# Kernel tuning notes

Measured on AMD Instinct MI355X. Metric: run time of the kernel, lower is better.

## Reference

```python
import jax, jax.numpy as jnp
import numpy as np

N_NODES = 50000
N_EDGES = 1600000
HIDDEN = 128
IN_DIM = 3  # x (1) + relative pos (2)


def setup_inputs() -> dict:
    key = jax.random.key(0)
    ks = jax.random.split(key, 5)
    x = jax.random.normal(ks[0], (N_NODES, 1), dtype=jnp.float32)
    pos = jax.random.normal(ks[1], (N_NODES, 2), dtype=jnp.float32)
    # MLP params (Linear(3,128) -> ReLU -> Linear(128,128)), fan-in scaled
    W1 = jax.random.normal(ks[2], (IN_DIM, HIDDEN), dtype=jnp.float32) / np.sqrt(IN_DIM)
    b1 = jnp.zeros((HIDDEN,), dtype=jnp.float32)
    W2 = jax.random.normal(ks[3], (HIDDEN, HIDDEN), dtype=jnp.float32) / np.sqrt(HIDDEN)
    b2 = jnp.zeros((HIDDEN,), dtype=jnp.float32)
    edge_index = jax.random.randint(ks[4], (2, N_EDGES), 0, N_NODES, dtype=jnp.int64)
    return {"x": x, "pos": pos, "W1": W1, "b1": b1, "W2": W2, "b2": b2,
            "edge_index": edge_index}


def reference(x, pos, W1, b1, W2, b2, edge_index):
    # PTConv with aggr='add': per-edge message = nn(cat([x_j, pos_j - pos_i]))
    # then scatter-add into destination node i.
    src = edge_index[0]  # j (neighbor / source)
    dst = edge_index[1]  # i (center / destination)
    msg_in = jnp.concatenate([x[src], pos[src] - pos[dst]], axis=-1)  # [E, 3]
    h = jax.nn.relu(msg_in @ W1 + b1) @ W2 + b2                        # [E, 128]
    out = jax.ops.segment_sum(h, dst, num_segments=x.shape[0])        # [N, 128]
    return out
```

## Files before the change

kernel.cpp:

```cpp
#include <hip/hip_runtime.h>


#define HIDDEN 128
#define BNODES 32
#define SUPSH 10
#define CAPA 36864
#define CAPF 1536
#define EPBA 2048
#define KSUB 16
#define CAP 1536
#define W2LD 136

typedef float v2f __attribute__((ext_vector_type(2)));
typedef short bf16x8 __attribute__((ext_vector_type(8)));
typedef float f32x4 __attribute__((ext_vector_type(4)));

__device__ __forceinline__ unsigned short f2bf(float f) {
    unsigned int u = __float_as_uint(f);
    u += 0x7fffu + ((u >> 16) & 1u);
    return (unsigned short)(u >> 16);
}

__global__ void k_init(int* __restrict__ bcurA, int* __restrict__ bcurF,
                       int NSUP, int NB) {
    int i = blockIdx.x * blockDim.x + threadIdx.x;
    if (i < NSUP) bcurA[i] = i * CAPA;
    if (i < NB)   bcurF[i] = i * CAPF;
}

__global__ __launch_bounds__(256) void k_scatA(const int* __restrict__ src,
                                               const int* __restrict__ dst,
                                               int* __restrict__ bcurA,
                                               unsigned int* __restrict__ pairsA,
                                               int E, int NSUP) {
    __shared__ int h[64];
    __shared__ int hb[64];
    int tid = threadIdx.x;
    if (tid < 64) h[tid] = 0;
    __syncthreads();
    int base = blockIdx.x * EPBA;
    int lim = base + EPBA; if (lim > E) lim = E;
    for (int i = base + tid; i < lim; i += 256) atomicAdd(&h[dst[i] >> SUPSH], 1);
    __syncthreads();
    if (tid < NSUP) {
        int c = h[tid];
        hb[tid] = c ? atomicAdd(&bcurA[tid], c) : 0;
        h[tid] = 0;
    }
    __syncthreads();
    for (int i = base + tid; i < lim; i += 256) {
        int d = dst[i];
        int s = d >> SUPSH;
        int loc = atomicAdd(&h[s], 1);
        int slot = hb[s] + loc;
        if (slot < (s + 1) * CAPA)
            pairsA[slot] = ((unsigned int)src[i] << SUPSH) | (unsigned int)(d & 1023);
    }
}

__global__ __launch_bounds__(256) void k_scatB(const int* __restrict__ bcurA,
                                               const unsigned int* __restrict__ pairsA,
                                               int* __restrict__ bcurF,
                                               unsigned int* __restrict__ pairsF,
                                               int NB) {
    __shared__ int h[32];
    __shared__ int hb[32];
    int tid = threadIdx.x;
    int s = blockIdx.x / KSUB;
    int k = blockIdx.x % KSUB;
    int base0 = s * CAPA;
    int ec = bcurA[s] - base0; if (ec > CAPA) ec = CAPA;
    int slice = (ec + KSUB - 1) / KSUB;
    int lo = base0 + k * slice;
    int hi = lo + slice; { int e1 = base0 + ec; if (hi > e1) hi = e1; }
    if (tid < 32) h[tid] = 0;
    __syncthreads();
    for (int i = lo + tid; i < hi; i += 256) atomicAdd(&h[(pairsA[i] >> 5) & 31u], 1);
    __syncthreads();
    if (tid < 32) {
        int c = h[tid];
        hb[tid] = c ? atomicAdd(&bcurF[s * 32 + tid], c) : 0;
        h[tid] = 0;
    }
    __syncthreads();
    for (int i = lo + tid; i < hi; i += 256) {
        unsigned int e = pairsA[i];
        int fbl = (int)((e >> 5) & 31u);
        int fb = s * 32 + fbl;
        int loc = atomicAdd(&h[fbl], 1);
        int slot = hb[fbl] + loc;
        if (slot < (fb + 1) * CAPF)
            pairsF[slot] = ((e >> SUPSH) << 5) | (e & 31u);
    }
}

__global__ __launch_bounds__(256) void k_main(const float* __restrict__ x,
                                              const float* __restrict__ pos,
                                              const float* __restrict__ W1,
                                              const float* __restrict__ b1,
                                              const int* __restrict__ bcurF,
                                              const unsigned int* __restrict__ pairs,
                                              float* __restrict__ agg,
                                              int* __restrict__ deg, int N) {
    __shared__ float4 f_s[CAP];
    __shared__ int cnt[BNODES];
    __shared__ int offn[BNODES + 1];
    __shared__ int cur[BNODES];

    int tid = threadIdx.x, lane = tid & 63, w = tid >> 6;
    int b = blockIdx.x;
    int n0 = b * BNODES;
    int e0 = b * CAPF;
    int ec = bcurF[b] - e0; if (ec > CAPF) ec = CAPF;
    int e1 = e0 + ec;

    int c0 = 2 * lane;
    v2f w10 = { W1[c0],              W1[c0 + 1] };
    v2f w11 = { W1[HIDDEN + c0],     W1[HIDDEN + c0 + 1] };
    v2f w12 = { W1[2 * HIDDEN + c0], W1[2 * HIDDEN + c0 + 1] };
    v2f b1v = { b1[c0], b1[c0 + 1] };
    const v2f zero = { 0.f, 0.f };
    const float2* pos2 = (const float2*)pos;

    v2f acc[8];
    int dga[8];
    #pragma unroll
    for (int s = 0; s < 8; ++s) { acc[s] = zero; dga[s] = 0; }

    for (int cbeg = e0; cbeg < e1; cbeg += CAP) {
        int ccnt = e1 - cbeg; if (ccnt > CAP) ccnt = CAP;
        if (tid < BNODES) cnt[tid] = 0;
        __syncthreads();
        for (int i = tid; i < ccnt; i += 256) atomicAdd(&cnt[pairs[cbeg + i] & 31u], 1);
        __syncthreads();
        if (tid < BNODES) {
            int v = cnt[tid];
            int sc = v;
            #pragma unroll
            for (int d = 1; d < BNODES; d <<= 1) {
                int u = __shfl_up(sc, d);
                if (lane >= d) sc += u;
            }
            offn[tid + 1] = sc;
            if (tid == 0) offn[0] = 0;
            cur[tid] = sc - v;
        }
        __syncthreads();
        for (int i = tid; i < ccnt; i += 256) {
            unsigned int r = pairs[cbeg + i];
            int j = (int)(r >> 5);
            int local = (int)(r & 31u);
            float a = x[j];
            float2 pj = pos2[j];
            float2 pi = pos2[n0 + local];
            int p = atomicAdd(&cur[local], 1);
            f_s[p] = make_float4(a, pj.x - pi.x, pj.y - pi.y, 0.f);
        }
        __syncthreads();
        #pragma unroll
        for (int s = 0; s < 8; ++s) {
            int l = w * 8 + s;
            int sb = offn[l], se = offn[l + 1];
            if (sb < se) {
                dga[s] += se - sb;
                v2f A = acc[s];
                #pragma unroll 4
                for (int t = sb; t < se; ++t) {
                    float4 f = f_s[t];
                    v2f h = f.x * w10 + b1v;
                    h = f.y * w11 + h;
                    h = f.z * w12 + h;
                    h = __builtin_elementwise_max(h, zero);
                    A += h;
                }
                acc[s] = A;
            }
        }
        __syncthreads();
    }

    #pragma unroll
    for (int s = 0; s < 8; ++s) {
        int l = w * 8 + s;
        int node = n0 + l;
        if (node < N) {
            ((v2f*)&agg[(size_t)node * HIDDEN])[lane] = acc[s];
            if (lane == 0) deg[node] = dga[s];
        }
    }
}

__global__ __launch_bounds__(256) void k_w2(float* __restrict__ agg,
                                            const float* __restrict__ W2,
                                            const float* __restrict__ b2,
                                            const int* __restrict__ deg, int N) {
    __shared__ unsigned short w2t[HIDDEN * W2LD];
    int tid = threadIdx.x;
    for (int idx = tid; idx < HIDDEN * HIDDEN; idx += 256) {
        int k = idx >> 7, c = idx & 127;
        w2t[c * W2LD + k] = f2bf(W2[idx]);
    }
    __syncthreads();

    int lane = tid & 63, w = tid >> 6;
    int row0 = blockIdx.x * 64 + w * 16;
    if (row0 >= N) return;

    int rA = row0 + (lane & 15);
    int koff = (lane >> 4) * 8;
    bool okA = rA < N;

    bf16x8 a[4];
    #pragma unroll
    for (int k0 = 0; k0 < 4; ++k0) {
        float4 fa = {0.f,0.f,0.f,0.f}, fb = {0.f,0.f,0.f,0.f};
        if (okA) {
            const float4* p = (const float4*)&agg[(size_t)rA * HIDDEN + k0 * 32 + koff];
            fa = p[0]; fb = p[1];
        }
        bf16x8 v;
        v[0] = (short)f2bf(fa.x); v[1] = (short)f2bf(fa.y);
        v[2] = (short)f2bf(fa.z); v[3] = (short)f2bf(fa.w);
        v[4] = (short)f2bf(fb.x); v[5] = (short)f2bf(fb.y);
        v[6] = (short)f2bf(fb.z); v[7] = (short)f2bf(fb.w);
        a[k0] = v;
    }

    f32x4 acc[8];
    #pragma unroll
    for (int ct = 0; ct < 8; ++ct) acc[ct] = (f32x4){0.f,0.f,0.f,0.f};

    #pragma unroll
    for (int ct = 0; ct < 8; ++ct) {
        int col = ct * 16 + (lane & 15);
        #pragma unroll
        for (int k0 = 0; k0 < 4; ++k0) {
            bf16x8 bfrag = *(const bf16x8*)&w2t[col * W2LD + k0 * 32 + koff];
            acc[ct] = __builtin_amdgcn_mfma_f32_16x16x32_bf16(a[k0], bfrag, acc[ct], 0, 0, 0);
        }
    }

    int mbase = row0 + (lane >> 4) * 4;
    float dg[4];
    #pragma unroll
    for (int i = 0; i < 4; ++i) dg[i] = (mbase + i < N) ? (float)deg[mbase + i] : 0.f;

    #pragma unroll
    for (int ct = 0; ct < 8; ++ct) {
        int col = ct * 16 + (lane & 15);
        float b2c = b2[col];
        #pragma unroll
        for (int i = 0; i < 4; ++i) {
            int r = mbase + i;
            if (r < N) agg[(size_t)r * HIDDEN + col] = acc[ct][i] + dg[i] * b2c;
        }
    }
}

extern "C" void kernel_launch(void* const* d_in, const int* in_sizes, int n_in,
                              void* d_out, int out_size, void* d_ws, size_t ws_size,
                              hipStream_t stream) {
    const float* x   = (const float*)d_in[0];
    const float* pos = (const float*)d_in[1];
    const float* W1  = (const float*)d_in[2];
    const float* b1  = (const float*)d_in[3];
    const float* W2  = (const float*)d_in[4];
    const float* b2  = (const float*)d_in[5];
    const int*   ei  = (const int*)d_in[6];

    int N = in_sizes[0];
    int E = in_sizes[6] / 2;
    const int* src = ei;
    const int* dst = ei + E;
    float* out = (float*)d_out;

    int NB   = (N + BNODES - 1) / BNODES;
    int NSUP = (N + 1023) >> SUPSH;

    int* bcurA = (int*)d_ws;
    int* bcurF = bcurA + 64;
    int* deg   = bcurF + NB;
    unsigned int* pairsA = (unsigned int*)(deg + N);
    unsigned int* pairsF = pairsA + (size_t)NSUP * CAPA;

    int gribsA = (E + EPBA - 1) / EPBA;

    k_init<<<(NB + 255) / 256, 256, 0, stream>>>(bcurA, bcurF, NSUP, NB);
    k_scatA<<<gribsA, 256, 0, stream>>>(src, dst, bcurA, pairsA, E, NSUP);
    k_scatB<<<NSUP * KSUB, 256, 0, stream>>>(bcurA, pairsA, bcurF, pairsF, NB);
    k_main<<<NB, 256, 0, stream>>>(x, pos, W1, b1, bcurF, pairsF, out, deg, N);
    k_w2<<<(N + 63) / 64, 256, 0, stream>>>(out, W2, b2, deg, N);
}
```

Measured before the change: 106.5 us.

## Replace init kernel with memset, batch pair loads, use readlane broadcast in edge MLP

The bucket cursors now start at zero through a memset rather than a separate init kernel, and slot indices become relative to each bucket. In k_main each thread loads its up to six pairs into registers once and reuses them for both the count and the fill pass, which removes the second global read. The per-edge first-layer loop now reads features once per lane and broadcasts them with readlane, replacing repeated LDS float4 reads. The readlane loop is serial across up to 64 edges, and the register-held pairs assume CAP is at most 6*256.

```diff
diff --git a/kernel.cpp b/kernel.cpp
--- a/kernel.cpp
+++ b/kernel.cpp
@@ -15,17 +15,14 @@
 typedef short bf16x8 __attribute__((ext_vector_type(8)));
 typedef float f32x4 __attribute__((ext_vector_type(4)));
 
+__device__ __forceinline__ float bcast(float v, int l) {
+    return __uint_as_float(__builtin_amdgcn_readlane(__float_as_uint(v), l));
+}
+
 __device__ __forceinline__ unsigned short f2bf(float f) {
     unsigned int u = __float_as_uint(f);
     u += 0x7fffu + ((u >> 16) & 1u);
     return (unsigned short)(u >> 16);
-}
-
-__global__ void k_init(int* __restrict__ bcurA, int* __restrict__ bcurF,
-                       int NSUP, int NB) {
-    int i = blockIdx.x * blockDim.x + threadIdx.x;
-    if (i < NSUP) bcurA[i] = i * CAPA;
-    if (i < NB)   bcurF[i] = i * CAPF;
 }
 
 __global__ __launch_bounds__(256) void k_scatA(const int* __restrict__ src,
@@ -51,10 +48,9 @@
     for (int i = base + tid; i < lim; i += 256) {
         int d = dst[i];
         int s = d >> SUPSH;
-        int loc = atomicAdd(&h[s], 1);
-        int slot = hb[s] + loc;
-        if (slot < (s + 1) * CAPA)
-            pairsA[slot] = ((unsigned int)src[i] << SUPSH) | (unsigned int)(d & 1023);
+        int loc = hb[s] + atomicAdd(&h[s], 1);
+        if (loc < CAPA)
+            pairsA[s * CAPA + loc] = ((unsigned int)src[i] << SUPSH) | (unsigned int)(d & 1023);
     }
 }
 
@@ -69,7 +65,7 @@
     int s = blockIdx.x / KSUB;
     int k = blockIdx.x % KSUB;
     int base0 = s * CAPA;
-    int ec = bcurA[s] - base0; if (ec > CAPA) ec = CAPA;
+    int ec = bcurA[s]; if (ec > CAPA) ec = CAPA;
     int slice = (ec + KSUB - 1) / KSUB;
     int lo = base0 + k * slice;
     int hi = lo + slice; { int e1 = base0 + ec; if (hi > e1) hi = e1; }
@@ -87,10 +83,9 @@
         unsigned int e = pairsA[i];
         int fbl = (int)((e >> 5) & 31u);
         int fb = s * 32 + fbl;
-        int loc = atomicAdd(&h[fbl], 1);
-        int slot = hb[fbl] + loc;
-        if (slot < (fb + 1) * CAPF)
-            pairsF[slot] = ((e >> SUPSH) << 5) | (e & 31u);
+        int loc = hb[fbl] + atomicAdd(&h[fbl], 1);
+        if (loc < CAPF)
+            pairsF[(size_t)fb * CAPF + loc] = ((e >> SUPSH) << 5) | (e & 31u);
     }
 }
 
@@ -111,7 +106,7 @@
     int b = blockIdx.x;
     int n0 = b * BNODES;
     int e0 = b * CAPF;
-    int ec = bcurF[b] - e0; if (ec > CAPF) ec = CAPF;
+    int ec = bcurF[b]; if (ec > CAPF) ec = CAPF;
     int e1 = e0 + ec;
 
     int c0 = 2 * lane;
@@ -131,7 +126,19 @@
         int ccnt = e1 - cbeg; if (ccnt > CAP) ccnt = CAP;
         if (tid < BNODES) cnt[tid] = 0;
         __syncthreads();
-        for (int i = tid; i < ccnt; i += 256) atomicAdd(&cnt[pairs[cbeg + i] & 31u], 1);
+        unsigned int rr0 = 0, rr1 = 0, rr2 = 0, rr3 = 0, rr4 = 0, rr5 = 0;
+        if (tid + 0 * 256 < ccnt) rr0 = pairs[cbeg + tid + 0 * 256];
+        if (tid + 1 * 256 < ccnt) rr1 = pairs[cbeg + tid + 1 * 256];
+        if (tid + 2 * 256 < ccnt) rr2 = pairs[cbeg + tid + 2 * 256];
+        if (tid + 3 * 256 < ccnt) rr3 = pairs[cbeg + tid + 3 * 256];
+        if (tid + 4 * 256 < ccnt) rr4 = pairs[cbeg + tid + 4 * 256];
+        if (tid + 5 * 256 < ccnt) rr5 = pairs[cbeg + tid + 5 * 256];
+        if (tid + 0 * 256 < ccnt) atomicAdd(&cnt[rr0 & 31u], 1);
+        if (tid + 1 * 256 < ccnt) atomicAdd(&cnt[rr1 & 31u], 1);
+        if (tid + 2 * 256 < ccnt) atomicAdd(&cnt[rr2 & 31u], 1);
+        if (tid + 3 * 256 < ccnt) atomicAdd(&cnt[rr3 & 31u], 1);
+        if (tid + 4 * 256 < ccnt) atomicAdd(&cnt[rr4 & 31u], 1);
+        if (tid + 5 * 256 < ccnt) atomicAdd(&cnt[rr5 & 31u], 1);
         __syncthreads();
         if (tid < BNODES) {
             int v = cnt[tid];
@@ -146,35 +153,43 @@
             cur[tid] = sc - v;
         }
         __syncthreads();
-        for (int i = tid; i < ccnt; i += 256) {
-            unsigned int r = pairs[cbeg + i];
-            int j = (int)(r >> 5);
-            int local = (int)(r & 31u);
-            float a = x[j];
-            float2 pj = pos2[j];
-            float2 pi = pos2[n0 + local];
-            int p = atomicAdd(&cur[local], 1);
-            f_s[p] = make_float4(a, pj.x - pi.x, pj.y - pi.y, 0.f);
+        #pragma unroll
+        for (int q = 0; q < 6; ++q) {
+            unsigned int r = q == 0 ? rr0 : q == 1 ? rr1 : q == 2 ? rr2
+                           : q == 3 ? rr3 : q == 4 ? rr4 : rr5;
+            if (tid + q * 256 < ccnt) {
+                int j = (int)(r >> 5);
+                int local = (int)(r & 31u);
+                float a = x[j];
+                float2 pj = pos2[j];
+                float2 pi = pos2[n0 + local];
+                int p = atomicAdd(&cur[local], 1);
+                f_s[p] = make_float4(a, pj.x - pi.x, pj.y - pi.y, 0.f);
+            }
         }
         __syncthreads();
         #pragma unroll
         for (int s = 0; s < 8; ++s) {
             int l = w * 8 + s;
             int sb = offn[l], se = offn[l + 1];
-            if (sb < se) {
-                dga[s] += se - sb;
-                v2f A = acc[s];
-                #pragma unroll 4
-                for (int t = sb; t < se; ++t) {
-                    float4 f = f_s[t];
-                    v2f h = f.x * w10 + b1v;
-                    h = f.y * w11 + h;
-                    h = f.z * w12 + h;
+            dga[s] += se - sb;
+            v2f A = acc[s];
+            for (int t0 = sb; t0 < se; t0 += 64) {
+                int m = se - t0; if (m > 64) m = 64;
+                float4 f = make_float4(0.f, 0.f, 0.f, 0.f);
+                if (lane < m) f = f_s[t0 + lane];
+                for (int e = 0; e < m; ++e) {
+                    float ae  = bcast(f.x, e);
+                    float rxe = bcast(f.y, e);
+                    float rye = bcast(f.z, e);
+                    v2f h = ae * w10 + b1v;
+                    h = rxe * w11 + h;
+                    h = rye * w12 + h;
                     h = __builtin_elementwise_max(h, zero);
                     A += h;
                 }
-                acc[s] = A;
             }
+            acc[s] = A;
         }
         __syncthreads();
     }
@@ -285,7 +300,7 @@
 
     int gribsA = (E + EPBA - 1) / EPBA;
 
-    k_init<<<(NB + 255) / 256, 256, 0, stream>>>(bcurA, bcurF, NSUP, NB);
+    hipMemsetAsync(bcurA, 0, (64 + (size_t)NB) * sizeof(int), stream);
     k_scatA<<<gribsA, 256, 0, stream>>>(src, dst, bcurA, pairsA, E, NSUP);
     k_scatB<<<NSUP * KSUB, 256, 0, stream>>>(bcurA, pairsA, bcurF, pairsF, NB);
     k_main<<<NB, 256, 0, stream>>>(x, pos, W1, b1, bcurF, pairsF, out, deg, N);
```

Measured after the change: 126.1 us. 1.18x slower.
